# Performance work log

Hardware: AMD Instinct MI355X
Metric: run time of the kernel (lower is better)

## Reference

```python
import jax, jax.numpy as jnp
import numpy as np

B, C, N, L, LAYERS = 32, 128, 307, 12, 4
LH = L + 1  # high-frequency channel time length after left-pad
BN_EPS = 1e-5


def _temporal_attention(seq, c1w, c2w, w, b, v, gamma, beta):
    # seq: [B, C, N, T]
    # conv1 (1x1 over channel dim) -> f1: [B, T, N]
    f1 = jnp.einsum('bcnt,c->btn', seq, c1w)
    # conv2 (1x1 over node dim)    -> f2: [B, T, C]
    f2 = jnp.einsum('bcnt,n->btc', seq, c2w)
    # scores = sigmoid(f1 @ w @ f2^T + b): [B, T, T]
    f1w = jnp.einsum('btn,nc->btc', f1, w)
    scores = jax.nn.sigmoid(jnp.einsum('btc,bqc->btq', f1w, f2) + b)
    # learned mixing: v @ scores
    logits = jnp.einsum('tk,bkq->btq', v, scores)
    # BatchNorm1d over tem_size channels (channel = last axis q after the
    # permute(0,2,1) in the torch code); training-mode batch statistics
    mean = logits.mean(axis=(0, 1), keepdims=True)
    var = ((logits - mean) ** 2).mean(axis=(0, 1), keepdims=True)
    logits = (logits - mean) * jax.lax.rsqrt(var + BN_EPS) * gamma + beta
    coefs = jax.nn.softmax(logits, axis=-1)  # [B, T, Q]
    # x_1 = einsum('bcnl,blq->bcnq', seq, coefs^T)
    return jnp.einsum('bcnt,bqt->bcnq', seq, coefs)


def _make_params(key, c, n, t, layers):
    ks = jax.random.split(key, 4)
    return dict(
        c1=jax.random.normal(ks[0], (layers, c), jnp.float32) * 0.05,
        c2=jax.random.normal(ks[1], (layers, n), jnp.float32) * 0.05,
        w=jax.random.normal(ks[2], (layers, n, c), jnp.float32) * 0.05,
        b=jnp.zeros((layers, t, t), jnp.float32),
        v=jax.random.normal(ks[3], (layers, t, t), jnp.float32) * 0.2,
        g=jnp.ones((layers, t), jnp.float32),
        beta=jnp.zeros((layers, t), jnp.float32),
    )


def setup_inputs():
    key = jax.random.key(0)
    k0, k1, k2, k3 = jax.random.split(key, 4)
    XL = jax.random.normal(k0, (B, C, N, L), jnp.float32)
    XH = jax.random.normal(k1, (B, C, N, L), jnp.float32)
    low = _make_params(k2, C, N, L, LAYERS)
    high = _make_params(k3, C, N, LH, LAYERS)
    return {
        'XL': XL, 'XH': XH,
        'low_c1': low['c1'], 'low_c2': low['c2'], 'low_w': low['w'],
        'low_b': low['b'], 'low_v': low['v'], 'low_g': low['g'], 'low_beta': low['beta'],
        'high_c1': high['c1'], 'high_c2': high['c2'], 'high_w': high['w'],
        'high_b': high['b'], 'high_v': high['v'], 'high_g': high['g'], 'high_beta': high['beta'],
        'alpha': jnp.array(-5.0, jnp.float32),
    }


def reference(XL, XH, low_c1, low_c2, low_w, low_b, low_v, low_g, low_beta,
              high_c1, high_c2, high_w, high_b, high_v, high_g, high_beta, alpha):
    res_xl, res_xh = XL, XH
    x = XL
    for i in range(LAYERS):
        x = _temporal_attention(x, low_c1[i], low_c2[i], low_w[i], low_b[i],
                                low_v[i], low_g[i], low_beta[i])
    xl = (res_xl[..., -1] + x[..., -1])[..., None]  # [B, C, N, 1]

    y = jnp.pad(XH, ((0, 0), (0, 0), (0, 0), (1, 0)))  # left-pad time -> [B,C,N,L+1]
    for i in range(LAYERS):
        y = _temporal_attention(y, high_c1[i], high_c2[i], high_w[i], high_b[i],
                                high_v[i], high_g[i], high_beta[i])
    xh = (res_xh[..., -1] + y[..., -1])[..., None]  # [B, C, N, 1]

    a = jax.nn.sigmoid(alpha)
    return a * xl + (1.0 - a) * xh
```

## Files before the change

### kernel.cpp

```cpp
#include <hip/hip_runtime.h>

#define Bn 32
#define Cc 128
#define Nn 307
#define Ll 12
#define LH 13
#define LAYERS 4
#define BN_EPS 1e-5f
#define SCW (Cc + 1)

__global__ __launch_bounds__(256) void k_g1(const float* __restrict__ XL,
                                            const float* __restrict__ XH,
                                            const float* __restrict__ lc1,
                                            const float* __restrict__ hc1,
                                            float* __restrict__ G1) {
    __shared__ float s_c1[LAYERS * Cc];
    __shared__ float sred[48 * 257];
    int tile = blockIdx.x;
    int b = blockIdx.y;
    int ch = blockIdx.z;
    const float* X = ch ? XH : XL;
    const float* c1 = ch ? hc1 : lc1;
    int tid = threadIdx.x;
    for (int j = tid; j < LAYERS * Cc; j += 256) s_c1[j] = c1[j];
    __syncthreads();
    int nl = tid & 31;
    int chunk = tid >> 5;
    int n = tile * 32 + nl;
    float acc[48];
#pragma unroll
    for (int j = 0; j < 48; ++j) acc[j] = 0.f;
    if (n < Nn) {
        const float* px = X + ((size_t)(b * Cc + chunk * 16) * Nn + n) * Ll;
#pragma unroll 2
        for (int i = 0; i < 16; ++i) {
            float4 v0 = *(const float4*)(px);
            float4 v1 = *(const float4*)(px + 4);
            float4 v2 = *(const float4*)(px + 8);
            float xv[12] = {v0.x, v0.y, v0.z, v0.w, v1.x, v1.y,
                            v1.z, v1.w, v2.x, v2.y, v2.z, v2.w};
            int c = chunk * 16 + i;
#pragma unroll
            for (int l = 0; l < LAYERS; ++l) {
                float wv = s_c1[l * Cc + c];
#pragma unroll
                for (int t = 0; t < 12; ++t) acc[l * 12 + t] += xv[t] * wv;
            }
            px += (size_t)Nn * Ll;
        }
    }
#pragma unroll
    for (int j = 0; j < 48; ++j) sred[j * 257 + tid] = acc[j];
    __syncthreads();
    size_t cb = (size_t)ch * LAYERS * Bn * (LH * Nn);
    for (int o = tid; o < 1536; o += 256) {
        int onl = o & 31, j = o >> 5;
        float v = 0.f;
#pragma unroll
        for (int k = 0; k < 8; ++k) v += sred[j * 257 + k * 32 + onl];
        int nn = tile * 32 + onl;
        if (nn < Nn) {
            int l = j / 12, t = j % 12;
            int t0 = ch ? (t + 1) : t;
            G1[cb + ((size_t)l * Bn + b) * (LH * Nn) + (size_t)t0 * Nn + nn] = v;
        }
    }
    if (tid < 128) {
        int l = tid >> 5, onl = tid & 31;
        int nn = tile * 32 + onl;
        int t0z = ch ? 0 : (LH - 1);
        if (nn < Nn)
            G1[cb + ((size_t)l * Bn + b) * (LH * Nn) + (size_t)t0z * Nn + nn] = 0.f;
    }
}

__global__ __launch_bounds__(256) void k_g2(const float* __restrict__ XL,
                                            const float* __restrict__ XH,
                                            const float* __restrict__ lc2,
                                            const float* __restrict__ hc2,
                                            float* __restrict__ G2) {
    __shared__ float s_c2[LAYERS * Nn];
    __shared__ float sred[4 * 48 * 65];
    int ctile = blockIdx.x;
    int b = blockIdx.y;
    int ch = blockIdx.z;
    const float* X = ch ? XH : XL;
    const float* c2 = ch ? hc2 : lc2;
    int tid = threadIdx.x;
    for (int j = tid; j < LAYERS * Nn; j += 256) s_c2[j] = c2[j];
    __syncthreads();
    int w = tid >> 6, lane = tid & 63;
    int c = ctile * 4 + w;
    float acc[48];
#pragma unroll
    for (int j = 0; j < 48; ++j) acc[j] = 0.f;
    const float* pb = X + (size_t)(b * Cc + c) * Nn * Ll;
    for (int k = 0; k < 5; ++k) {
        int n = k * 64 + lane;
        if (n < Nn) {
            const float* px = pb + (size_t)n * Ll;
            float4 v0 = *(const float4*)(px);
            float4 v1 = *(const float4*)(px + 4);
            float4 v2 = *(const float4*)(px + 8);
            float xv[12] = {v0.x, v0.y, v0.z, v0.w, v1.x, v1.y,
                            v1.z, v1.w, v2.x, v2.y, v2.z, v2.w};
#pragma unroll
            for (int l = 0; l < LAYERS; ++l) {
                float wv = s_c2[l * Nn + n];
#pragma unroll
                for (int t = 0; t < 12; ++t) acc[l * 12 + t] += xv[t] * wv;
            }
        }
    }
#pragma unroll
    for (int j = 0; j < 48; ++j) sred[(w * 48 + j) * 65 + lane] = acc[j];
    __syncthreads();
    size_t cb = (size_t)ch * LAYERS * Bn * (LH * Cc);
    if (tid < 192) {
        int ww = tid / 48, j = tid % 48;
        float v = 0.f;
        for (int k2 = 0; k2 < 64; ++k2) v += sred[(ww * 48 + j) * 65 + k2];
        int l = j / 12, t = j % 12;
        int t0 = ch ? (t + 1) : t;
        int cc2 = ctile * 4 + ww;
        G2[cb + ((size_t)l * Bn + b) * (LH * Cc) + (size_t)t0 * Cc + cc2] = v;
    } else if (ch && tid < 208) {
        int r = tid - 192;
        int l = r >> 2, ww = r & 3;
        G2[cb + ((size_t)l * Bn + b) * (LH * Cc) + ctile * 4 + ww] = 0.f;
    }
}

#define GWR 4
__global__ __launch_bounds__(256) void k_gw(const float* __restrict__ lw,
                                            const float* __restrict__ hw,
                                            const float* __restrict__ G1,
                                            float* __restrict__ GW) {
    __shared__ float sG1[GWR * Nn];
    __shared__ float sred[8][GWR][Cc];
    int tile = blockIdx.x;
    int chl = blockIdx.y;
    int ch = chl >> 2, l = chl & 3;
    const float* w = (ch ? hw : lw) + (size_t)l * Nn * Cc;
    const float* g1 = G1 + (size_t)chl * Bn * (LH * Nn) + (size_t)tile * GWR * Nn;
    int tid = threadIdx.x;
    for (int i = tid; i < GWR * Nn / 4; i += 256)
        ((float4*)sG1)[i] = ((const float4*)g1)[i];
    __syncthreads();
    int c4 = (tid & 31) * 4;
    int stripe = tid >> 5;
    float4 a0 = {0.f, 0.f, 0.f, 0.f}, a1 = a0, a2 = a0, a3 = a0;
#define GW_FMA(wv, nn)                                         \
    {                                                          \
        float g0 = sG1[0 * Nn + (nn)];                         \
        float g1v = sG1[1 * Nn + (nn)];                        \
        float g2v = sG1[2 * Nn + (nn)];                        \
        float g3v = sG1[3 * Nn + (nn)];                        \
        a0.x += wv.x * g0;  a0.y += wv.y * g0;                 \
        a0.z += wv.z * g0;  a0.w += wv.w * g0;                 \
        a1.x += wv.x * g1v; a1.y += wv.y * g1v;                \
        a1.z += wv.z * g1v; a1.w += wv.w * g1v;                \
        a2.x += wv.x * g2v; a2.y += wv.y * g2v;                \
        a2.z += wv.z * g2v; a2.w += wv.w * g2v;                \
        a3.x += wv.x * g3v; a3.y += wv.y * g3v;                \
        a3.z += wv.z * g3v; a3.w += wv.w * g3v;                \
    }
    int n = stripe;
    for (; n + 24 < Nn; n += 32) {
        float4 w0 = *(const float4*)(w + (size_t)n * Cc + c4);
        float4 w1 = *(const float4*)(w + (size_t)(n + 8) * Cc + c4);
        float4 w2 = *(const float4*)(w + (size_t)(n + 16) * Cc + c4);
        float4 w3 = *(const float4*)(w + (size_t)(n + 24) * Cc + c4);
        GW_FMA(w0, n);
        GW_FMA(w1, n + 8);
        GW_FMA(w2, n + 16);
        GW_FMA(w3, n + 24);
    }
    for (; n < Nn; n += 8) {
        float4 w0 = *(const float4*)(w + (size_t)n * Cc + c4);
        GW_FMA(w0, n);
    }
#undef GW_FMA
    *(float4*)&sred[stripe][0][c4] = a0;
    *(float4*)&sred[stripe][1][c4] = a1;
    *(float4*)&sred[stripe][2][c4] = a2;
    *(float4*)&sred[stripe][3][c4] = a3;
    __syncthreads();
    float* out = GW + (size_t)chl * Bn * (LH * Cc) + (size_t)tile * GWR * Cc;
    for (int o = tid; o < GWR * Cc; o += 256) {
        int r = o >> 7, cc = o & 127;
        float v = 0.f;
#pragma unroll
        for (int s = 0; s < 8; ++s) v += sred[s][r][cc];
        out[o] = v;
    }
}

__global__ __launch_bounds__(256) void k_m(const float* __restrict__ GW,
                                           const float* __restrict__ G2,
                                           float* __restrict__ M) {
    __shared__ float sGW[LH][SCW];
    __shared__ float sG2[LH][SCW];
    int blk = blockIdx.x;
    int ch = blk >> 7;
    int T = ch ? LH : Ll;
    const float* gw = GW + (size_t)blk * (LH * Cc);
    const float* g2 = G2 + (size_t)blk * (LH * Cc);
    int tid = threadIdx.x;
    for (int i = tid; i < LH * Cc; i += 256) {
        int t = i >> 7, c = i & 127;
        sGW[t][c] = gw[i];
        sG2[t][c] = g2[i];
    }
    __syncthreads();
    float* Mo = M + (size_t)blk * (LH * LH);
    for (int i = tid; i < T * T; i += 256) {
        int t0 = i / T, t1 = i % T;
        float a = 0.f;
#pragma unroll 8
        for (int cc = 0; cc < Cc; ++cc) a += sGW[t0][cc] * sG2[t1][cc];
        Mo[t0 * LH + t1] = a;
    }
}

template <int T>
__device__ __forceinline__ void first_impl(int ch, int b,
                                           const float* __restrict__ M,
                                           const float* __restrict__ bb,
                                           const float* __restrict__ v,
                                           float* __restrict__ Lg,
                                           float* __restrict__ Stats) {
    const int TT = T * T;
    __shared__ float sS[LH * LH];
    __shared__ float sA[LH * LH];
    int tid = threadIdx.x;
    const float* Ml = M + ((size_t)(ch * LAYERS + 0) * Bn + b) * (LH * LH);
    if (tid < TT) {
        int t = tid / T, q = tid % T;
        float a = bb[tid] + Ml[t * LH + q];
        sS[tid] = 1.f / (1.f + expf(-a));
    }
    __syncthreads();
    if (tid < TT) {
        int t = tid / T, q = tid % T;
        float a = 0.f;
#pragma unroll
        for (int k = 0; k < T; ++k) a += v[t * T + k] * sS[k * T + q];
        sA[tid] = a;
        Lg[(size_t)(ch * Bn + b) * (LH * LH) + tid] = a;
    }
    __syncthreads();
    if (tid < T) {
        float s = 0.f, ss = 0.f;
#pragma unroll
        for (int t = 0; t < T; ++t) {
            float x = sA[t * T + tid];
            s += x;
            ss += x * x;
        }
        float* St = Stats + (size_t)(0 * 2 + ch) * 2 * (LH * Bn);
        St[tid * Bn + b] = s;
        St[LH * Bn + tid * Bn + b] = ss;
    }
}

__global__ __launch_bounds__(192) void k_first(const float* __restrict__ M,
                                               const float* __restrict__ lb,
                                               const float* __restrict__ lv,
                                               const float* __restrict__ hb,
                                               const float* __restrict__ hv,
                                               float* __restrict__ Lg,
                                               float* __restrict__ Stats) {
    int ch = blockIdx.x >> 5, b = blockIdx.x & 31;
    if (ch == 0)
        first_impl<Ll>(0, b, M, lb, lv, Lg, Stats);
    else
        first_impl<LH>(1, b, M, hb, hv, Lg, Stats);
}

template <int T>
__device__ __forceinline__ void mid_impl(int ch, int b, int l,
                                         const float* __restrict__ M,
                                         const float* __restrict__ bb_all,
                                         const float* __restrict__ v_all,
                                         const float* __restrict__ g_all,
                                         const float* __restrict__ be_all,
                                         float* __restrict__ Lg,
                                         float* __restrict__ Stats,
                                         float* __restrict__ Pws) {
    const int TT = T * T;
    __shared__ float sP[LH * LH], sC[LH * LH], sA[LH * LH], sB[LH * LH], sM[LH * LH];
    __shared__ float sMean[LH], sScale[LH], sShift[LH];
    int tid = threadIdx.x;
    bool first = (l == 0);
    float* Lgb = Lg + (size_t)(ch * Bn + b) * (LH * LH);
    float* Pb = Pws + (size_t)(ch * Bn + b) * (LH * LH);
    if (tid < T) {
        const float* St = Stats + (size_t)(l * 2 + ch) * 2 * (LH * Bn);
        float s = 0.f, ss = 0.f;
        for (int b2 = 0; b2 < Bn; ++b2) {
            s += St[tid * Bn + b2];
            ss += St[LH * Bn + tid * Bn + b2];
        }
        float inv = 1.f / (float)(Bn * T);
        float m = s * inv;
        float var = ss * inv - m * m;
        sMean[tid] = m;
        sScale[tid] = rsqrtf(var + BN_EPS) * g_all[l * T + tid];
        sShift[tid] = be_all[l * T + tid];
    }
    if (tid < TT) {
        sA[tid] = Lgb[tid];
        if (!first) sP[tid] = Pb[tid];
    }
    __syncthreads();
    if (tid < T) {
        float vals[T];
        float mx = -1e30f;
#pragma unroll
        for (int q = 0; q < T; ++q) {
            float x = (sA[tid * T + q] - sMean[q]) * sScale[q] + sShift[q];
            vals[q] = x;
            mx = fmaxf(mx, x);
        }
        float sm = 0.f;
#pragma unroll
        for (int q = 0; q < T; ++q) {
            vals[q] = expf(vals[q] - mx);
            sm += vals[q];
        }
        float inv = 1.f / sm;
#pragma unroll
        for (int q = 0; q < T; ++q) sC[tid * T + q] = vals[q] * inv;
    }
    __syncthreads();
    if (tid < TT) {
        int t0 = tid / T, q = tid % T;
        float a;
        if (first) {
            a = sC[q * T + t0];
        } else {
            a = 0.f;
#pragma unroll
            for (int t = 0; t < T; ++t) a += sP[t0 * T + t] * sC[q * T + t];
        }
        sB[tid] = a;
        Pb[tid] = a;
    }
    const float* Mn = M + ((size_t)(ch * LAYERS + l + 1) * Bn + b) * (LH * LH);
    for (int i = tid; i < T * LH; i += 192) sM[i] = Mn[i];
    __syncthreads();
    if (tid < TT) {
        int t = tid / T, t1 = tid % T;
        float a = 0.f;
#pragma unroll
        for (int t0 = 0; t0 < T; ++t0) a += sB[t0 * T + t] * sM[t0 * LH + t1];
        sA[tid] = a;
    }
    __syncthreads();
    const float* bbn = bb_all + (size_t)(l + 1) * TT;
    if (tid < TT) {
        int t = tid / T, q = tid % T;
        float a = bbn[tid];
#pragma unroll
        for (int t1 = 0; t1 < T; ++t1) a += sA[t * T + t1] * sB[t1 * T + q];
        sP[tid] = 1.f / (1.f + expf(-a));
    }
    __syncthreads();
    const float* vn = v_all + (size_t)(l + 1) * TT;
    if (tid < TT) {
        int t = tid / T, q = tid % T;
        float a = 0.f;
#pragma unroll
        for (int k = 0; k < T; ++k) a += vn[t * T + k] * sP[k * T + q];
        sA[tid] = a;
        Lgb[tid] = a;
    }
    __syncthreads();
    if (tid < T) {
        float s = 0.f, ss = 0.f;
#pragma unroll
        for (int t = 0; t < T; ++t) {
            float x = sA[t * T + tid];
            s += x;
            ss += x * x;
        }
        float* St = Stats + (size_t)((l + 1) * 2 + ch) * 2 * (LH * Bn);
        St[tid * Bn + b] = s;
        St[LH * Bn + tid * Bn + b] = ss;
    }
}

__global__ __launch_bounds__(192) void k_mid(const float* __restrict__ M,
                                             const float* __restrict__ lb,
                                             const float* __restrict__ lv,
                                             const float* __restrict__ lgam,
                                             const float* __restrict__ lbet,
                                             const float* __restrict__ hb,
                                             const float* __restrict__ hv,
                                             const float* __restrict__ hgam,
                                             const float* __restrict__ hbet,
                                             float* __restrict__ Lg,
                                             float* __restrict__ Stats,
                                             float* __restrict__ Pws, int l) {
    int ch = blockIdx.x >> 5, b = blockIdx.x & 31;
    if (ch == 0)
        mid_impl<Ll>(0, b, l, M, lb, lv, lgam, lbet, Lg, Stats, Pws);
    else
        mid_impl<LH>(1, b, l, M, hb, hv, hgam, hbet, Lg, Stats, Pws);
}

template <int T>
__device__ __forceinline__ void last_impl(int ch, int b,
                                          const float* __restrict__ g_all,
                                          const float* __restrict__ be_all,
                                          const float* __restrict__ Lg,
                                          const float* __restrict__ Stats,
                                          const float* __restrict__ Pws,
                                          float* __restrict__ Pcol) {
    const int TT = T * T;
    const int l = LAYERS - 1;
    __shared__ float sP[LH * LH], sC[LH * LH], sA[LH * LH], sB[LH * LH];
    __shared__ float sMean[LH], sScale[LH], sShift[LH];
    int tid = threadIdx.x;
    const float* Lgb = Lg + (size_t)(ch * Bn + b) * (LH * LH);
    const float* Pb = Pws + (size_t)(ch * Bn + b) * (LH * LH);
    if (tid < T) {
        const float* St = Stats + (size_t)(l * 2 + ch) * 2 * (LH * Bn);
        float s = 0.f, ss = 0.f;
        for (int b2 = 0; b2 < Bn; ++b2) {
            s += St[tid * Bn + b2];
            ss += St[LH * Bn + tid * Bn + b2];
        }
        float inv = 1.f / (float)(Bn * T);
        float m = s * inv;
        float var = ss * inv - m * m;
        sMean[tid] = m;
        sScale[tid] = rsqrtf(var + BN_EPS) * g_all[l * T + tid];
        sShift[tid] = be_all[l * T + tid];
    }
    if (tid < TT) {
        sA[tid] = Lgb[tid];
        sP[tid] = Pb[tid];
    }
    __syncthreads();
    if (tid < T) {
        float vals[T];
        float mx = -1e30f;
#pragma unroll
        for (int q = 0; q < T; ++q) {
            float x = (sA[tid * T + q] - sMean[q]) * sScale[q] + sShift[q];
            vals[q] = x;
            mx = fmaxf(mx, x);
        }
        float sm = 0.f;
#pragma unroll
        for (int q = 0; q < T; ++q) {
            vals[q] = expf(vals[q] - mx);
            sm += vals[q];
        }
        float inv = 1.f / sm;
#pragma unroll
        for (int q = 0; q < T; ++q) sC[tid * T + q] = vals[q] * inv;
    }
    __syncthreads();
    if (tid < TT) {
        int t0 = tid / T, q = tid % T;
        float a = 0.f;
#pragma unroll
        for (int t = 0; t < T; ++t) a += sP[t0 * T + t] * sC[q * T + t];
        sB[tid] = a;
    }
    __syncthreads();
    if (tid < T) Pcol[(size_t)ch * Bn * LH + b * LH + tid] = sB[tid * T + (T - 1)];
}

__global__ __launch_bounds__(192) void k_last(const float* __restrict__ lgam,
                                              const float* __restrict__ lbet,
                                              const float* __restrict__ hgam,
                                              const float* __restrict__ hbet,
                                              const float* __restrict__ Lg,
                                              const float* __restrict__ Stats,
                                              const float* __restrict__ Pws,
                                              float* __restrict__ Pcol) {
    int ch = blockIdx.x >> 5, b = blockIdx.x & 31;
    if (ch == 0)
        last_impl<Ll>(0, b, lgam, lbet, Lg, Stats, Pws, Pcol);
    else
        last_impl<LH>(1, b, hgam, hbet, Lg, Stats, Pws, Pcol);
}

__global__ __launch_bounds__(256) void k_final(const float* __restrict__ XL,
                                               const float* __restrict__ XH,
                                               const float* __restrict__ Pcol,
                                               const float* __restrict__ alpha,
                                               float* __restrict__ out) {
    __shared__ float s_pl[Ll];
    __shared__ float s_ph[LH];
    int b = blockIdx.y;
    int tid = threadIdx.x;
    if (tid < Ll) s_pl[tid] = Pcol[b * LH + tid];
    if (tid < LH) s_ph[tid] = Pcol[Bn * LH + b * LH + tid];
    __syncthreads();
    int cn = blockIdx.x * blockDim.x + tid;
    if (cn >= Cc * Nn) return;
    size_t idx = (size_t)b * Cc * Nn + cn;
    const float* pl = XL + idx * Ll;
    const float* ph = XH + idx * Ll;
    float accL = 0.f, accH = 0.f;
#pragma unroll
    for (int t = 0; t < Ll; ++t) {
        accL += pl[t] * s_pl[t];
        accH += ph[t] * s_ph[t + 1];
    }
    float a = 1.f / (1.f + expf(-alpha[0]));
    float xl = pl[Ll - 1] + accL;
    float xh = ph[Ll - 1] + accH;
    out[idx] = a * xl + (1.f - a) * xh;
}

extern "C" void kernel_launch(void* const* d_in, const int* in_sizes, int n_in,
                              void* d_out, int out_size, void* d_ws, size_t ws_size,
                              hipStream_t stream) {
    const float* XL = (const float*)d_in[0];
    const float* XH = (const float*)d_in[1];
    const float* lc1 = (const float*)d_in[2];
    const float* lc2 = (const float*)d_in[3];
    const float* lw = (const float*)d_in[4];
    const float* lb = (const float*)d_in[5];
    const float* lv = (const float*)d_in[6];
    const float* lg = (const float*)d_in[7];
    const float* lbeta = (const float*)d_in[8];
    const float* hc1 = (const float*)d_in[9];
    const float* hc2 = (const float*)d_in[10];
    const float* hw = (const float*)d_in[11];
    const float* hb = (const float*)d_in[12];
    const float* hv = (const float*)d_in[13];
    const float* hg = (const float*)d_in[14];
    const float* hbeta = (const float*)d_in[15];
    const float* alpha = (const float*)d_in[16];
    float* out = (float*)d_out;

    float* ws = (float*)d_ws;
    float* G1 = ws;
    float* G2 = G1 + (size_t)2 * LAYERS * Bn * LH * Nn;
    float* M = G2 + (size_t)2 * LAYERS * Bn * LH * Cc;
    float* Pcol = M + (size_t)2 * LAYERS * Bn * LH * LH;
    float* Stats = Pcol + (size_t)2 * Bn * LH;
    float* Lg = Stats + (size_t)4 * LAYERS * LH * Bn;
    float* Pws = Lg + (size_t)2 * Bn * LH * LH;
    float* GW = Pws + (size_t)2 * Bn * LH * LH;

    k_g1<<<dim3(10, 32, 2), 256, 0, stream>>>(XL, XH, lc1, hc1, G1);
    k_g2<<<dim3(32, 32, 2), 256, 0, stream>>>(XL, XH, lc2, hc2, G2);
    k_gw<<<dim3(104, 8), 256, 0, stream>>>(lw, hw, G1, GW);
    k_m<<<256, 256, 0, stream>>>(GW, G2, M);
    k_first<<<64, 192, 0, stream>>>(M, lb, lv, hb, hv, Lg, Stats);
    k_mid<<<64, 192, 0, stream>>>(M, lb, lv, lg, lbeta, hb, hv, hg, hbeta, Lg, Stats, Pws, 0);
    k_mid<<<64, 192, 0, stream>>>(M, lb, lv, lg, lbeta, hb, hv, hg, hbeta, Lg, Stats, Pws, 1);
    k_mid<<<64, 192, 0, stream>>>(M, lb, lv, lg, lbeta, hb, hv, hg, hbeta, Lg, Stats, Pws, 2);
    k_last<<<64, 192, 0, stream>>>(lg, lbeta, hg, hbeta, Lg, Stats, Pws, Pcol);
    k_final<<<dim3((Cc * Nn + 255) / 256, Bn), 256, 0, stream>>>(XL, XH, Pcol, alpha, out);
}
```

Before: 254.5 us.

## Split k_g1 channel reduction across two blocks and use wave shuffles for reductions

k_g1 now splits the 128-channel reduction into two halves across twice as many blocks. Each half writes a separate partial G1 buffer, and k_gw sums the two partials while loading its tile. Both k_g1 and k_g2 replace most of their shared-memory reductions with __shfl_xor wave reductions, which shrinks LDS use and may improve occupancy. The cost is double the G1 workspace, extra G1 write and read traffic, and more register pressure from the shuffles.

Result: no change. 252.7 us (-0.7%).

```diff
diff --git a/kernel.cpp b/kernel.cpp
--- a/kernel.cpp
+++ b/kernel.cpp
@@ -8,6 +8,7 @@
 #define LAYERS 4
 #define BN_EPS 1e-5f
 #define SCW (Cc + 1)
+#define G1SZ ((size_t)2 * LAYERS * Bn * LH * Nn)
 
 __global__ __launch_bounds__(256) void k_g1(const float* __restrict__ XL,
                                             const float* __restrict__ XH,
@@ -15,8 +16,10 @@
                                             const float* __restrict__ hc1,
                                             float* __restrict__ G1) {
     __shared__ float s_c1[LAYERS * Cc];
-    __shared__ float sred[48 * 257];
-    int tile = blockIdx.x;
+    __shared__ float sred[48 * 132];
+    int bx = blockIdx.x;
+    int tile = bx % 10;
+    int csplit = bx / 10;
     int b = blockIdx.y;
     int ch = blockIdx.z;
     const float* X = ch ? XH : XL;
@@ -31,15 +34,15 @@
 #pragma unroll
     for (int j = 0; j < 48; ++j) acc[j] = 0.f;
     if (n < Nn) {
-        const float* px = X + ((size_t)(b * Cc + chunk * 16) * Nn + n) * Ll;
-#pragma unroll 2
-        for (int i = 0; i < 16; ++i) {
+        const float* px = X + ((size_t)(b * Cc + csplit * 64 + chunk * 8) * Nn + n) * Ll;
+#pragma unroll 4
+        for (int i = 0; i < 8; ++i) {
             float4 v0 = *(const float4*)(px);
             float4 v1 = *(const float4*)(px + 4);
             float4 v2 = *(const float4*)(px + 8);
             float xv[12] = {v0.x, v0.y, v0.z, v0.w, v1.x, v1.y,
                             v1.z, v1.w, v2.x, v2.y, v2.z, v2.w};
-            int c = chunk * 16 + i;
+            int c = csplit * 64 + chunk * 8 + i;
 #pragma unroll
             for (int l = 0; l < LAYERS; ++l) {
                 float wv = s_c1[l * Cc + c];
@@ -50,19 +53,24 @@
         }
     }
 #pragma unroll
-    for (int j = 0; j < 48; ++j) sred[j * 257 + tid] = acc[j];
-    __syncthreads();
+    for (int j = 0; j < 48; ++j) acc[j] += __shfl_xor(acc[j], 32, 64);
+    int w = tid >> 6;
+    if ((tid & 32) == 0) {
+#pragma unroll
+        for (int j = 0; j < 48; ++j) sred[j * 132 + w * 32 + nl] = acc[j];
+    }
+    __syncthreads();
+    float* G1o = G1 + (size_t)csplit * G1SZ;
     size_t cb = (size_t)ch * LAYERS * Bn * (LH * Nn);
     for (int o = tid; o < 1536; o += 256) {
         int onl = o & 31, j = o >> 5;
-        float v = 0.f;
-#pragma unroll
-        for (int k = 0; k < 8; ++k) v += sred[j * 257 + k * 32 + onl];
+        float v = sred[j * 132 + onl] + sred[j * 132 + 32 + onl] +
+                  sred[j * 132 + 64 + onl] + sred[j * 132 + 96 + onl];
         int nn = tile * 32 + onl;
         if (nn < Nn) {
             int l = j / 12, t = j % 12;
             int t0 = ch ? (t + 1) : t;
-            G1[cb + ((size_t)l * Bn + b) * (LH * Nn) + (size_t)t0 * Nn + nn] = v;
+            G1o[cb + ((size_t)l * Bn + b) * (LH * Nn) + (size_t)t0 * Nn + nn] = v;
         }
     }
     if (tid < 128) {
@@ -70,7 +78,7 @@
         int nn = tile * 32 + onl;
         int t0z = ch ? 0 : (LH - 1);
         if (nn < Nn)
-            G1[cb + ((size_t)l * Bn + b) * (LH * Nn) + (size_t)t0z * Nn + nn] = 0.f;
+            G1o[cb + ((size_t)l * Bn + b) * (LH * Nn) + (size_t)t0z * Nn + nn] = 0.f;
     }
 }
 
@@ -80,7 +88,7 @@
                                             const float* __restrict__ hc2,
                                             float* __restrict__ G2) {
     __shared__ float s_c2[LAYERS * Nn];
-    __shared__ float sred[4 * 48 * 65];
+    __shared__ float sred[4][48][9];
     int ctile = blockIdx.x;
     int b = blockIdx.y;
     int ch = blockIdx.z;
@@ -95,6 +103,7 @@
 #pragma unroll
     for (int j = 0; j < 48; ++j) acc[j] = 0.f;
     const float* pb = X + (size_t)(b * Cc + c) * Nn * Ll;
+#pragma unroll
     for (int k = 0; k < 5; ++k) {
         int n = k * 64 + lane;
         if (n < Nn) {
@@ -113,13 +122,23 @@
         }
     }
 #pragma unroll
-    for (int j = 0; j < 48; ++j) sred[(w * 48 + j) * 65 + lane] = acc[j];
+    for (int j = 0; j < 48; ++j) acc[j] += __shfl_xor(acc[j], 1, 64);
+#pragma unroll
+    for (int j = 0; j < 48; ++j) acc[j] += __shfl_xor(acc[j], 2, 64);
+#pragma unroll
+    for (int j = 0; j < 48; ++j) acc[j] += __shfl_xor(acc[j], 4, 64);
+    if ((lane & 7) == 0) {
+        int s = lane >> 3;
+#pragma unroll
+        for (int j = 0; j < 48; ++j) sred[w][j][s] = acc[j];
+    }
     __syncthreads();
     size_t cb = (size_t)ch * LAYERS * Bn * (LH * Cc);
     if (tid < 192) {
         int ww = tid / 48, j = tid % 48;
         float v = 0.f;
-        for (int k2 = 0; k2 < 64; ++k2) v += sred[(ww * 48 + j) * 65 + k2];
+#pragma unroll
+        for (int s = 0; s < 8; ++s) v += sred[ww][j][s];
         int l = j / 12, t = j % 12;
         int t0 = ch ? (t + 1) : t;
         int cc2 = ctile * 4 + ww;
@@ -142,10 +161,15 @@
     int chl = blockIdx.y;
     int ch = chl >> 2, l = chl & 3;
     const float* w = (ch ? hw : lw) + (size_t)l * Nn * Cc;
-    const float* g1 = G1 + (size_t)chl * Bn * (LH * Nn) + (size_t)tile * GWR * Nn;
-    int tid = threadIdx.x;
-    for (int i = tid; i < GWR * Nn / 4; i += 256)
-        ((float4*)sG1)[i] = ((const float4*)g1)[i];
+    size_t g1off = (size_t)chl * Bn * (LH * Nn) + (size_t)tile * GWR * Nn;
+    const float4* g1a = (const float4*)(G1 + g1off);
+    const float4* g1b = (const float4*)(G1 + G1SZ + g1off);
+    int tid = threadIdx.x;
+    for (int i = tid; i < GWR * Nn / 4; i += 256) {
+        float4 pa = g1a[i], pb = g1b[i];
+        float4 s = {pa.x + pb.x, pa.y + pb.y, pa.z + pb.z, pa.w + pb.w};
+        ((float4*)sG1)[i] = s;
+    }
     __syncthreads();
     int c4 = (tid & 31) * 4;
     int stripe = tid >> 5;
@@ -543,7 +567,7 @@
 
     float* ws = (float*)d_ws;
     float* G1 = ws;
-    float* G2 = G1 + (size_t)2 * LAYERS * Bn * LH * Nn;
+    float* G2 = G1 + 2 * G1SZ;
     float* M = G2 + (size_t)2 * LAYERS * Bn * LH * Cc;
     float* Pcol = M + (size_t)2 * LAYERS * Bn * LH * LH;
     float* Stats = Pcol + (size_t)2 * Bn * LH;
@@ -551,7 +575,7 @@
     float* Pws = Lg + (size_t)2 * Bn * LH * LH;
     float* GW = Pws + (size_t)2 * Bn * LH * LH;
 
-    k_g1<<<dim3(10, 32, 2), 256, 0, stream>>>(XL, XH, lc1, hc1, G1);
+    k_g1<<<dim3(20, 32, 2), 256, 0, stream>>>(XL, XH, lc1, hc1, G1);
     k_g2<<<dim3(32, 32, 2), 256, 0, stream>>>(XL, XH, lc2, hc2, G2);
     k_gw<<<dim3(104, 8), 256, 0, stream>>>(lw, hw, G1, GW);
     k_m<<<256, 256, 0, stream>>>(GW, G2, M);
```

## Split layer dimension across threads in G1/G2 reduction kernels to cut registers

Applied to the files above, without the earlier changes.

k_g1 and k_g2 now assign one layer per thread, so each thread keeps 12 accumulators instead of 48. This shrinks shared-memory reduction buffers and, with launch_bounds(256,4), targets higher occupancy. Grids are retiled to 16 nodes per block for g1 and 8 channels per block for g2. The trade-off is that each X element is now loaded by four threads, one per layer, relying on cache hits instead of register reuse.

New measurement: 272.9 us. 7.2% more time.

```diff
diff --git a/kernel.cpp b/kernel.cpp
--- a/kernel.cpp
+++ b/kernel.cpp
@@ -8,14 +8,16 @@
 #define LAYERS 4
 #define BN_EPS 1e-5f
 #define SCW (Cc + 1)
-
-__global__ __launch_bounds__(256) void k_g1(const float* __restrict__ XL,
-                                            const float* __restrict__ XH,
-                                            const float* __restrict__ lc1,
-                                            const float* __restrict__ hc1,
-                                            float* __restrict__ G1) {
+#define G1SZ ((size_t)2 * LAYERS * Bn * LH * Nn)
+
+#define NT1 16
+__global__ __launch_bounds__(256, 4) void k_g1(const float* __restrict__ XL,
+                                               const float* __restrict__ XH,
+                                               const float* __restrict__ lc1,
+                                               const float* __restrict__ hc1,
+                                               float* __restrict__ G1) {
     __shared__ float s_c1[LAYERS * Cc];
-    __shared__ float sred[48 * 257];
+    __shared__ float sred[12 * 260];
     int tile = blockIdx.x;
     int b = blockIdx.y;
     int ch = blockIdx.z;
@@ -24,63 +26,60 @@
     int tid = threadIdx.x;
     for (int j = tid; j < LAYERS * Cc; j += 256) s_c1[j] = c1[j];
     __syncthreads();
-    int nl = tid & 31;
-    int chunk = tid >> 5;
-    int n = tile * 32 + nl;
-    float acc[48];
-#pragma unroll
-    for (int j = 0; j < 48; ++j) acc[j] = 0.f;
+    int nl = tid & 15;
+    int l = (tid >> 4) & 3;
+    int cs = tid >> 6;
+    int n = tile * NT1 + nl;
+    float4 a0 = {0.f, 0.f, 0.f, 0.f}, a1 = a0, a2 = a0;
     if (n < Nn) {
-        const float* px = X + ((size_t)(b * Cc + chunk * 16) * Nn + n) * Ll;
-#pragma unroll 2
-        for (int i = 0; i < 16; ++i) {
+        const float* px = X + ((size_t)(b * Cc + cs * 32) * Nn + n) * Ll;
+        const float* wp = s_c1 + l * Cc + cs * 32;
+#pragma unroll 4
+        for (int cc = 0; cc < 32; ++cc) {
             float4 v0 = *(const float4*)(px);
             float4 v1 = *(const float4*)(px + 4);
             float4 v2 = *(const float4*)(px + 8);
-            float xv[12] = {v0.x, v0.y, v0.z, v0.w, v1.x, v1.y,
-                            v1.z, v1.w, v2.x, v2.y, v2.z, v2.w};
-            int c = chunk * 16 + i;
-#pragma unroll
-            for (int l = 0; l < LAYERS; ++l) {
-                float wv = s_c1[l * Cc + c];
-#pragma unroll
-                for (int t = 0; t < 12; ++t) acc[l * 12 + t] += xv[t] * wv;
-            }
+            float wv = wp[cc];
+            a0.x += v0.x * wv; a0.y += v0.y * wv; a0.z += v0.z * wv; a0.w += v0.w * wv;
+            a1.x += v1.x * wv; a1.y += v1.y * wv; a1.z += v1.z * wv; a1.w += v1.w * wv;
+            a2.x += v2.x * wv; a2.y += v2.y * wv; a2.z += v2.z * wv; a2.w += v2.w * wv;
             px += (size_t)Nn * Ll;
         }
     }
-#pragma unroll
-    for (int j = 0; j < 48; ++j) sred[j * 257 + tid] = acc[j];
-    __syncthreads();
-    size_t cb = (size_t)ch * LAYERS * Bn * (LH * Nn);
-    for (int o = tid; o < 1536; o += 256) {
-        int onl = o & 31, j = o >> 5;
-        float v = 0.f;
-#pragma unroll
-        for (int k = 0; k < 8; ++k) v += sred[j * 257 + k * 32 + onl];
-        int nn = tile * 32 + onl;
-        if (nn < Nn) {
-            int l = j / 12, t = j % 12;
-            int t0 = ch ? (t + 1) : t;
-            G1[cb + ((size_t)l * Bn + b) * (LH * Nn) + (size_t)t0 * Nn + nn] = v;
-        }
-    }
-    if (tid < 128) {
-        int l = tid >> 5, onl = tid & 31;
-        int nn = tile * 32 + onl;
+    int g = tid & 63;
+    float av[12] = {a0.x, a0.y, a0.z, a0.w, a1.x, a1.y,
+                    a1.z, a1.w, a2.x, a2.y, a2.z, a2.w};
+#pragma unroll
+    for (int t = 0; t < 12; ++t) sred[t * 260 + cs * 64 + g] = av[t];
+    __syncthreads();
+#pragma unroll
+    for (int r = 0; r < 3; ++r) {
+        int o = r * 256 + tid;
+        int og = o & 63, t = o >> 6;
+        float v = sred[t * 260 + og] + sred[t * 260 + 64 + og] +
+                  sred[t * 260 + 128 + og] + sred[t * 260 + 192 + og];
+        int onl = og & 15, ol = og >> 4;
+        int nn = tile * NT1 + onl;
+        int t0 = ch ? (t + 1) : t;
+        if (nn < Nn)
+            G1[((size_t)(ch * LAYERS + ol) * Bn + b) * (LH * Nn) + (size_t)t0 * Nn + nn] = v;
+    }
+    if (tid < 64) {
+        int onl = tid & 15, ol = tid >> 4;
+        int nn = tile * NT1 + onl;
         int t0z = ch ? 0 : (LH - 1);
         if (nn < Nn)
-            G1[cb + ((size_t)l * Bn + b) * (LH * Nn) + (size_t)t0z * Nn + nn] = 0.f;
-    }
-}
-
-__global__ __launch_bounds__(256) void k_g2(const float* __restrict__ XL,
-                                            const float* __restrict__ XH,
-                                            const float* __restrict__ lc2,
-                                            const float* __restrict__ hc2,
-                                            float* __restrict__ G2) {
+            G1[((size_t)(ch * LAYERS + ol) * Bn + b) * (LH * Nn) + (size_t)t0z * Nn + nn] = 0.f;
+    }
+}
+
+__global__ __launch_bounds__(256, 4) void k_g2(const float* __restrict__ XL,
+                                               const float* __restrict__ XH,
+                                               const float* __restrict__ lc2,
+                                               const float* __restrict__ hc2,
+                                               float* __restrict__ G2) {
     __shared__ float s_c2[LAYERS * Nn];
-    __shared__ float sred[4 * 48 * 65];
+    __shared__ float sred[12 * 260];
     int ctile = blockIdx.x;
     int b = blockIdx.y;
     int ch = blockIdx.z;
@@ -89,45 +88,47 @@
     int tid = threadIdx.x;
     for (int j = tid; j < LAYERS * Nn; j += 256) s_c2[j] = c2[j];
     __syncthreads();
-    int w = tid >> 6, lane = tid & 63;
-    int c = ctile * 4 + w;
-    float acc[48];
-#pragma unroll
-    for (int j = 0; j < 48; ++j) acc[j] = 0.f;
+    int c8 = tid & 7;
+    int l = (tid >> 3) & 3;
+    int ns = tid >> 5;
+    int c = ctile * 8 + c8;
+    float4 a0 = {0.f, 0.f, 0.f, 0.f}, a1 = a0, a2 = a0;
     const float* pb = X + (size_t)(b * Cc + c) * Nn * Ll;
-    for (int k = 0; k < 5; ++k) {
-        int n = k * 64 + lane;
-        if (n < Nn) {
-            const float* px = pb + (size_t)n * Ll;
-            float4 v0 = *(const float4*)(px);
-            float4 v1 = *(const float4*)(px + 4);
-            float4 v2 = *(const float4*)(px + 8);
-            float xv[12] = {v0.x, v0.y, v0.z, v0.w, v1.x, v1.y,
-                            v1.z, v1.w, v2.x, v2.y, v2.z, v2.w};
-#pragma unroll
-            for (int l = 0; l < LAYERS; ++l) {
-                float wv = s_c2[l * Nn + n];
-#pragma unroll
-                for (int t = 0; t < 12; ++t) acc[l * 12 + t] += xv[t] * wv;
-            }
-        }
-    }
-#pragma unroll
-    for (int j = 0; j < 48; ++j) sred[(w * 48 + j) * 65 + lane] = acc[j];
-    __syncthreads();
-    size_t cb = (size_t)ch * LAYERS * Bn * (LH * Cc);
-    if (tid < 192) {
-        int ww = tid / 48, j = tid % 48;
-        float v = 0.f;
-        for (int k2 = 0; k2 < 64; ++k2) v += sred[(ww * 48 + j) * 65 + k2];
-        int l = j / 12, t = j % 12;
-        int t0 = ch ? (t + 1) : t;
-        int cc2 = ctile * 4 + ww;
-        G2[cb + ((size_t)l * Bn + b) * (LH * Cc) + (size_t)t0 * Cc + cc2] = v;
-    } else if (ch && tid < 208) {
-        int r = tid - 192;
-        int l = r >> 2, ww = r & 3;
-        G2[cb + ((size_t)l * Bn + b) * (LH * Cc) + ctile * 4 + ww] = 0.f;
+    const float* wp = s_c2 + l * Nn;
+#pragma unroll 4
+    for (int n = ns; n < Nn; n += 8) {
+        const float* px = pb + (size_t)n * Ll;
+        float4 v0 = *(const float4*)(px);
+        float4 v1 = *(const float4*)(px + 4);
+        float4 v2 = *(const float4*)(px + 8);
+        float wv = wp[n];
+        a0.x += v0.x * wv; a0.y += v0.y * wv; a0.z += v0.z * wv; a0.w += v0.w * wv;
+        a1.x += v1.x * wv; a1.y += v1.y * wv; a1.z += v1.z * wv; a1.w += v1.w * wv;
+        a2.x += v2.x * wv; a2.y += v2.y * wv; a2.z += v2.z * wv; a2.w += v2.w * wv;
+    }
+    float av[12] = {a0.x, a0.y, a0.z, a0.w, a1.x, a1.y,
+                    a1.z, a1.w, a2.x, a2.y, a2.z, a2.w};
+#pragma unroll
+    for (int t = 0; t < 12; ++t) sred[t * 260 + tid] = av[t];
+    __syncthreads();
+    size_t cb;
+#pragma unroll
+    for (int r = 0; r < 2; ++r) {
+        int o = r * 256 + tid;
+        if (o < 384) {
+            int og = o & 31, t = o >> 5;
+            float v = 0.f;
+#pragma unroll
+            for (int s = 0; s < 8; ++s) v += sred[t * 260 + s * 32 + og];
+            int oc8 = og & 7, ol = og >> 3;
+            int t0 = ch ? (t + 1) : t;
+            G2[((size_t)(ch * LAYERS + ol) * Bn + b) * (LH * Cc) + (size_t)t0 * Cc +
+               ctile * 8 + oc8] = v;
+        }
+    }
+    if (ch && tid < 32) {
+        int oc8 = tid & 7, ol = tid >> 3;
+        G2[((size_t)(ch * LAYERS + ol) * Bn + b) * (LH * Cc) + ctile * 8 + oc8] = 0.f;
     }
 }
 
@@ -543,7 +544,7 @@
 
     float* ws = (float*)d_ws;
     float* G1 = ws;
-    float* G2 = G1 + (size_t)2 * LAYERS * Bn * LH * Nn;
+    float* G2 = G1 + G1SZ;
     float* M = G2 + (size_t)2 * LAYERS * Bn * LH * Cc;
     float* Pcol = M + (size_t)2 * LAYERS * Bn * LH * LH;
     float* Stats = Pcol + (size_t)2 * Bn * LH;
@@ -551,8 +552,8 @@
     float* Pws = Lg + (size_t)2 * Bn * LH * LH;
     float* GW = Pws + (size_t)2 * Bn * LH * LH;
 
-    k_g1<<<dim3(10, 32, 2), 256, 0, stream>>>(XL, XH, lc1, hc1, G1);
-    k_g2<<<dim3(32, 32, 2), 256, 0, stream>>>(XL, XH, lc2, hc2, G2);
+    k_g1<<<dim3(20, 32, 2), 256, 0, stream>>>(XL, XH, lc1, hc1, G1);
+    k_g2<<<dim3(16, 32, 2), 256, 0, stream>>>(XL, XH, lc2, hc2, G2);
     k_gw<<<dim3(104, 8), 256, 0, stream>>>(lw, hw, G1, GW);
     k_m<<<256, 256, 0, stream>>>(GW, G2, M);
     k_first<<<64, 192, 0, stream>>>(M, lb, lv, hb, hv, Lg, Stats);
```
